# Optimization experiments

Hardware: AMD Instinct MI355X
Metric: run time of the kernel (lower is better)

## Reference

```python
import jax, jax.numpy as jnp
import numpy as np

B, S, D, H = 2, 2048, 1024, 16
DK = D // H  # 64


def setup_inputs() -> dict:
    key = jax.random.key(0)
    ks = jax.random.split(key, 9)
    s = 0.02
    return {
        "embeddings": jax.random.normal(ks[0], (B, S, D), jnp.float32),
        "Wq": jax.random.normal(ks[1], (H, D, DK), jnp.float32) * s,
        "bq": jax.random.normal(ks[2], (H, DK), jnp.float32) * s,
        "Wk": jax.random.normal(ks[3], (H, D, DK), jnp.float32) * s,
        "bk": jax.random.normal(ks[4], (H, DK), jnp.float32) * s,
        "Wv": jax.random.normal(ks[5], (H, D, DK), jnp.float32) * s,
        "bv": jax.random.normal(ks[6], (H, DK), jnp.float32) * s,
        "Wo": jax.random.normal(ks[7], (D, D), jnp.float32) * s,
        "bo": jax.random.normal(ks[8], (D,), jnp.float32) * s,
    }


def reference(embeddings, Wq, bq, Wk, bk, Wv, bv, Wo, bo):
    b, s, d = embeddings.shape
    dk = Wq.shape[-1]
    # batched per-head projections: [b,s,d] x [h,d,k] -> [b,h,s,k]
    q = jnp.einsum('bsd,hdk->bhsk', embeddings, Wq) + bq[None, :, None, :]
    k = jnp.einsum('bsd,hdk->bhsk', embeddings, Wk) + bk[None, :, None, :]
    v = jnp.einsum('bsd,hdk->bhsk', embeddings, Wv) + bv[None, :, None, :]
    scores = jnp.einsum('bhqk,bhsk->bhqs', q, k) / jnp.sqrt(jnp.float32(dk))
    causal_mask = jnp.triu(jnp.ones((s, s), dtype=bool), k=1)  # True above diagonal
    scores = jnp.where(causal_mask, jnp.float32(-1e9), scores)
    weights = jax.nn.softmax(scores, axis=-1)
    ctx = jnp.einsum('bhqs,bhsk->bhqk', weights, v)
    concat = ctx.transpose(0, 2, 1, 3).reshape(b, s, d)  # head-major concat, matches torch.cat
    return concat @ Wo + bo
```

## Files before the change

kernel.cpp:

```cpp
#include <hip/hip_runtime.h>
#include <hip/hip_bf16.h>

typedef unsigned short u16;
typedef unsigned int u32;
typedef __bf16 bf16x8 __attribute__((ext_vector_type(8)));
typedef float f32x4 __attribute__((ext_vector_type(4)));
typedef float f32x16 __attribute__((ext_vector_type(16)));

#define AS1 __attribute__((address_space(1)))
#define AS3 __attribute__((address_space(3)))

#define NB 2
#define NS 2048
#define ND 1024
#define NH 16
#define NK 64

__device__ __forceinline__ u16 f2bf(float f) {
  u32 u = __builtin_bit_cast(u32, f);
  return (u16)((u + 0x7FFFu + ((u >> 16) & 1u)) >> 16);
}

__device__ __forceinline__ u32 cvt_pk_bf16(float lo, float hi) {
  u32 u;
  asm("v_cvt_pk_bf16_f32 %0, %1, %2" : "=v"(u) : "v"(lo), "v"(hi));
  return u;
}

__device__ __forceinline__ void stage_tile(u16* lds, const u16* __restrict__ src, int rs,
                                           int wid, int lane) {
#pragma unroll
  for (int i = 0; i < 2; ++i) {
    int c = wid * 128 + i * 64 + lane;
    int row = c >> 3;
    int kc = (c & 7) ^ (row & 7);
    __builtin_amdgcn_global_load_lds((const AS1 u32*)(src + (size_t)row * rs + kc * 8),
                                     (AS3 u32*)(lds + (wid * 128 + i * 64) * 8), 16, 0, 0);
  }
}

__device__ __forceinline__ void stage_warp(u16* lds, const u16* __restrict__ src, int rs,
                                           int lane) {
#pragma unroll
  for (int i = 0; i < 8; ++i) {
    int c = i * 64 + lane;
    int row = c >> 3;
    int kc = (c & 7) ^ (row & 7);
    __builtin_amdgcn_global_load_lds((const AS1 u32*)(src + (size_t)row * rs + kc * 8),
                                     (AS3 u32*)(lds + i * 512), 16, 0, 0);
  }
}

__device__ __forceinline__ bf16x8 read_slot(const u16* lds, int row, int slot) {
  return *(const bf16x8*)(lds + row * 64 + (slot ^ (row & 7)) * 8);
}

__device__ __forceinline__ bf16x8 read_frag(const u16* lds, int row, int ks, int lane) {
  int slot = ((lane >> 4) + ks * 4) ^ (row & 7);
  return *(const bf16x8*)(lds + row * 64 + slot * 8);
}

__global__ __launch_bounds__(256) void convert_kernel(const float* __restrict__ src,
                                                      u16* __restrict__ dst, int n) {
  int i = (blockIdx.x * 256 + threadIdx.x) * 4;
  if (i >= n) return;
  float4 v = *(const float4*)(src + i);
  u32 w0 = cvt_pk_bf16(v.x, v.y);
  u32 w1 = cvt_pk_bf16(v.z, v.w);
  uint2 w; w.x = w0; w.y = w1;
  *(uint2*)(dst + i) = w;
}

__global__ __launch_bounds__(256) void transpose_conv(const float* __restrict__ src,
                                                      u16* __restrict__ dst, int R, int C) {
  __shared__ float tile[32][33];
  size_t base = (size_t)blockIdx.z * R * C;
  src += base;
  dst += base;
  int c0 = blockIdx.x * 32, r0 = blockIdx.y * 32;
  int tx = threadIdx.x, ty = threadIdx.y;
#pragma unroll
  for (int i = 0; i < 4; ++i)
    tile[ty + 8 * i][tx] = src[(size_t)(r0 + ty + 8 * i) * C + c0 + tx];
  __syncthreads();
#pragma unroll
  for (int i = 0; i < 4; ++i)
    dst[(size_t)(c0 + ty + 8 * i) * R + r0 + tx] = f2bf(tile[tx][ty + 8 * i]);
}

template <int MODE>
__global__ __launch_bounds__(256) void gemm128(const u16* __restrict__ A,
                                               const u16* __restrict__ Bt,
                                               const float* __restrict__ b0,
                                               const float* __restrict__ b1,
                                               const float* __restrict__ b2,
                                               u16* __restrict__ Qo, u16* __restrict__ Ko,
                                               u16* __restrict__ Vo,
                                               float* __restrict__ out) {
  __shared__ alignas(16) u16 lds_a[128 * 64];
  __shared__ alignas(16) u16 lds_b[128 * 64];
  int tid = threadIdx.x, lane = tid & 63, wid = tid >> 6;
  int wm = wid >> 1, wn = wid & 1;
  int m0 = blockIdx.x * 128, n0 = blockIdx.y * 128;
  int col = lane & 15;
  f32x4 zero4 = {0.f, 0.f, 0.f, 0.f};
  f32x4 acc[4][4];
#pragma unroll
  for (int i = 0; i < 4; ++i)
#pragma unroll
    for (int j = 0; j < 4; ++j) acc[i][j] = zero4;
  for (int k0 = 0; k0 < ND; k0 += 64) {
    stage_tile(lds_a, A + (size_t)m0 * ND + k0, ND, wid, lane);
    stage_tile(lds_a + 4096, A + (size_t)(m0 + 64) * ND + k0, ND, wid, lane);
    stage_tile(lds_b, Bt + (size_t)n0 * ND + k0, ND, wid, lane);
    stage_tile(lds_b + 4096, Bt + (size_t)(n0 + 64) * ND + k0, ND, wid, lane);
    __syncthreads();
#pragma unroll
    for (int ks = 0; ks < 2; ++ks) {
      bf16x8 af[4], bf[4];
#pragma unroll
      for (int i = 0; i < 4; ++i) af[i] = read_frag(lds_a, wm * 64 + i * 16 + col, ks, lane);
#pragma unroll
      for (int j = 0; j < 4; ++j) bf[j] = read_frag(lds_b, wn * 64 + j * 16 + col, ks, lane);
#pragma unroll
      for (int i = 0; i < 4; ++i)
#pragma unroll
        for (int j = 0; j < 4; ++j)
          acc[i][j] = __builtin_amdgcn_mfma_f32_16x16x32_bf16(af[i], bf[j], acc[i][j], 0, 0, 0);
    }
    __syncthreads();
  }
  int rbase = m0 + wm * 64 + (lane >> 4) * 4;
#pragma unroll
  for (int j = 0; j < 4; ++j) {
    int n = n0 + wn * 64 + j * 16 + col;
    if constexpr (MODE == 0) {
      int which = n >> 10, hh = (n >> 6) & 15, dk = n & 63;
      const float* bp = which == 0 ? b0 : which == 1 ? b1 : b2;
      float bn = bp[hh * 64 + dk];
      if (which == 0) {
#pragma unroll
        for (int i = 0; i < 4; ++i)
#pragma unroll
          for (int r = 0; r < 4; ++r) {
            int m = rbase + i * 16 + r;
            int bb = m >> 11, s = m & (NS - 1);
            Qo[((size_t)(bb * NH + hh) * NS + s) * NK + dk] =
                f2bf((acc[i][j][r] + bn) * 0.18033688f);
          }
      } else if (which == 1) {
#pragma unroll
        for (int i = 0; i < 4; ++i)
#pragma unroll
          for (int r = 0; r < 4; ++r) {
            int m = rbase + i * 16 + r;
            int bb = m >> 11, s = m & (NS - 1);
            Ko[((size_t)(bb * NH + hh) * NS + s) * NK + dk] = f2bf(acc[i][j][r] + bn);
          }
      } else {
#pragma unroll
        for (int i = 0; i < 4; ++i)
#pragma unroll
          for (int r = 0; r < 4; ++r) {
            int m = rbase + i * 16 + r;
            int bb = m >> 11, s = m & (NS - 1);
            int ss = (s & ~12) | ((s & 4) << 1) | ((s & 8) >> 1);
            Vo[((size_t)(bb * NH + hh) * NK + dk) * NS + ss] = f2bf(acc[i][j][r] + bn);
          }
      }
    } else {
      float bn = b0[n];
#pragma unroll
      for (int i = 0; i < 4; ++i)
#pragma unroll
        for (int r = 0; r < 4; ++r)
          out[(size_t)(rbase + i * 16 + r) * ND + n] = acc[i][j][r] + bn;
    }
  }
}

__global__ __launch_bounds__(128, 2) void attn_kernel(const u16* __restrict__ Q,
                                                      const u16* __restrict__ K,
                                                      const u16* __restrict__ Vt,
                                                      u16* __restrict__ ctx) {
  __shared__ alignas(16) u16 lds[2][2][8192];
  __shared__ float slab[2][32];
  int tid = threadIdx.x, lane = tid & 63, w = tid >> 6;
  int hi = lane >> 5, ln = lane & 31;
  int bh = blockIdx.x;
  int pr = blockIdx.y;
  const u16* Qb = Q + bh * (NS * NK);
  const u16* Kb = K + bh * (NS * NK);
  const u16* Vb = Vt + bh * (NK * NS);
  int b = bh >> 4, h = bh & 15;
  u16* myK0 = &lds[w][0][0];
  u16* myV0 = &lds[w][0][4096];
  u16* myK1 = &lds[w][1][0];
  u16* myV1 = &lds[w][1][4096];

#pragma unroll 1
  for (int half = 0; half < 2; ++half) {
    int qt = half ? pr : (31 - pr);
    int q0w = qt * 64 + w * 32;
    int qg = q0w + ln;
    bf16x8 qf[4];
#pragma unroll
    for (int ks = 0; ks < 4; ++ks)
      qf[ks] = *(const bf16x8*)(Qb + qg * NK + ks * 16 + hi * 8);

    f32x16 acc0, acc1;
#pragma unroll
    for (int r = 0; r < 16; ++r) { acc0[r] = 0.f; acc1[r] = 0.f; }
    float lp = 0.f;
    int nt = qt + 1;

    stage_warp(myK0, Kb, NK, lane);
    stage_warp(myV0, Vb, NS, lane);
    if (nt > 1) {
      stage_warp(myK1, Kb + 64 * NK, NK, lane);
      stage_warp(myV1, Vb + 64, NS, lane);
    }

#pragma unroll 1
    for (int t = 0; t < nt; ++t) {
      const u16* lk = (t & 1) ? myK1 : myK0;
      const u16* lv = (t & 1) ? myV1 : myV0;
      if (t + 1 < nt) {
        asm volatile("s_waitcnt vmcnt(16)" ::: "memory");
      } else {
        asm volatile("s_waitcnt vmcnt(0)" ::: "memory");
      }
      __builtin_amdgcn_sched_barrier(0);
      f32x16 sc0, sc1;
#pragma unroll
      for (int r = 0; r < 16; ++r) { sc0[r] = 0.f; sc1[r] = 0.f; }
      __builtin_amdgcn_s_setprio(1);
#pragma unroll
      for (int ks = 0; ks < 4; ++ks) {
        bf16x8 kf0 = read_slot(lk, ln, 2 * ks + hi);
        sc0 = __builtin_amdgcn_mfma_f32_32x32x16_bf16(kf0, qf[ks], sc0, 0, 0, 0);
        bf16x8 kf1 = read_slot(lk, 32 + ln, 2 * ks + hi);
        sc1 = __builtin_amdgcn_mfma_f32_32x32x16_bf16(kf1, qf[ks], sc1, 0, 0, 0);
      }
      __builtin_amdgcn_s_setprio(0);
      if (t == qt) {
#pragma unroll
        for (int r = 0; r < 16; ++r) {
          int kl = t * 64 + (r & 3) + 8 * (r >> 2) + 4 * hi;
          if (kl > qg) sc0[r] = -1e30f;
          if (kl + 32 > qg) sc1[r] = -1e30f;
        }
      }
      float ps[4] = {0.f, 0.f, 0.f, 0.f};
#pragma unroll
      for (int r = 0; r < 16; ++r) {
        float p = exp2f(sc0[r]);
        sc0[r] = p;
        ps[r & 3] += p;
      }
#pragma unroll
      for (int r = 0; r < 16; ++r) {
        float p = exp2f(sc1[r]);
        sc1[r] = p;
        ps[r & 3] += p;
      }
      lp += (ps[0] + ps[1]) + (ps[2] + ps[3]);
      u32 wd[8];
      bf16x8 pa[4];
#pragma unroll
      for (int i = 0; i < 8; ++i) wd[i] = cvt_pk_bf16(sc0[2 * i], sc0[2 * i + 1]);
      { uint4 q4; q4.x = wd[0]; q4.y = wd[1]; q4.z = wd[2]; q4.w = wd[3];
        pa[0] = __builtin_bit_cast(bf16x8, q4);
        q4.x = wd[4]; q4.y = wd[5]; q4.z = wd[6]; q4.w = wd[7];
        pa[1] = __builtin_bit_cast(bf16x8, q4); }
#pragma unroll
      for (int i = 0; i < 8; ++i) wd[i] = cvt_pk_bf16(sc1[2 * i], sc1[2 * i + 1]);
      { uint4 q4; q4.x = wd[0]; q4.y = wd[1]; q4.z = wd[2]; q4.w = wd[3];
        pa[2] = __builtin_bit_cast(bf16x8, q4);
        q4.x = wd[4]; q4.y = wd[5]; q4.z = wd[6]; q4.w = wd[7];
        pa[3] = __builtin_bit_cast(bf16x8, q4); }
      __builtin_amdgcn_s_setprio(1);
#pragma unroll
      for (int ks = 0; ks < 4; ++ks) {
        bf16x8 vf0 = read_slot(lv, ln, 2 * ks + hi);
        acc0 = __builtin_amdgcn_mfma_f32_32x32x16_bf16(pa[ks], vf0, acc0, 0, 0, 0);
        bf16x8 vf1 = read_slot(lv, 32 + ln, 2 * ks + hi);
        acc1 = __builtin_amdgcn_mfma_f32_32x32x16_bf16(pa[ks], vf1, acc1, 0, 0, 0);
      }
      __builtin_amdgcn_s_setprio(0);
      if (t + 2 < nt) {
        asm volatile("s_waitcnt lgkmcnt(0)" ::: "memory");
        __builtin_amdgcn_sched_barrier(0);
        u16* nk = (t & 1) ? myK1 : myK0;
        u16* nv = (t & 1) ? myV1 : myV0;
        stage_warp(nk, Kb + (t + 2) * 64 * NK, NK, lane);
        stage_warp(nv, Vb + (t + 2) * 64, NS, lane);
      }
    }
    lp += __shfl_xor(lp, 32);
    if (!hi) slab[w][ln] = 1.0f / lp;
    float iv[16];
#pragma unroll
    for (int r = 0; r < 16; ++r) iv[r] = slab[w][(r & 3) + 8 * (r >> 2) + 4 * hi];
#pragma unroll
    for (int r = 0; r < 16; ++r) {
      int qq = q0w + (r & 3) + 8 * (r >> 2) + 4 * hi;
      size_t base = (size_t)(b * NS + qq) * ND + h * NK + ln;
      ctx[base] = f2bf(acc0[r] * iv[r]);
      ctx[base + 32] = f2bf(acc1[r] * iv[r]);
    }
  }
}

extern "C" void kernel_launch(void* const* d_in, const int* in_sizes, int n_in,
                              void* d_out, int out_size, void* d_ws, size_t ws_size,
                              hipStream_t stream) {
  (void)in_sizes; (void)n_in; (void)out_size;
  const float* emb = (const float*)d_in[0];
  const float* Wq = (const float*)d_in[1];
  const float* bq = (const float*)d_in[2];
  const float* Wk = (const float*)d_in[3];
  const float* bk = (const float*)d_in[4];
  const float* Wv = (const float*)d_in[5];
  const float* bv = (const float*)d_in[6];
  const float* Wo = (const float*)d_in[7];
  const float* bo = (const float*)d_in[8];
  float* out = (float*)d_out;

  const size_t EMB_N = (size_t)NB * NS * ND;
  const size_t W_N = (size_t)NH * ND * NK;
  const size_t QKV_N = (size_t)NB * NH * NS * NK;
  if (ws_size < (EMB_N + 4 * W_N + 3 * QKV_N) * sizeof(u16)) return;
  u16* ws = (u16*)d_ws;
  u16* emb_bf = ws;
  u16* Wqt = emb_bf + EMB_N;
  u16* Wkt = Wqt + W_N;
  u16* Wvt = Wkt + W_N;
  u16* Wot = Wvt + W_N;
  u16* Qb = Wot + W_N;
  u16* Kb = Qb + QKV_N;
  u16* Vtb = Kb + QKV_N;
  u16* ctxb = emb_bf;

  convert_kernel<<<dim3((int)(EMB_N / 4 / 256)), dim3(256), 0, stream>>>(emb, emb_bf,
                                                                         (int)EMB_N);
  dim3 tb(32, 8);
  transpose_conv<<<dim3(2, 32, 16), tb, 0, stream>>>(Wq, Wqt, ND, NK);
  transpose_conv<<<dim3(2, 32, 16), tb, 0, stream>>>(Wk, Wkt, ND, NK);
  transpose_conv<<<dim3(2, 32, 16), tb, 0, stream>>>(Wv, Wvt, ND, NK);
  transpose_conv<<<dim3(32, 32, 1), tb, 0, stream>>>(Wo, Wot, ND, ND);
  gemm128<0><<<dim3(32, 24), dim3(256), 0, stream>>>(emb_bf, Wqt, bq, bk, bv, Qb, Kb, Vtb,
                                                     nullptr);
  attn_kernel<<<dim3(32, 16), dim3(128), 0, stream>>>(Qb, Kb, Vtb, ctxb);
  gemm128<1><<<dim3(32, 8), dim3(256), 0, stream>>>(ctxb, Wot, bo, nullptr, nullptr,
                                                    nullptr, nullptr, nullptr, out);
}
```

Before: 141.6 us.

## Launch one block per query tile and load V fragments directly from global

Drops the paired heavy/light causal tile scheme: each block now handles a single query tile, and the grid doubles to 32x32 blocks. V is no longer staged in LDS. Each iteration loads V fragments straight from global memory into registers, which halves LDS use and shortens the vmcnt wait. The aim is more blocks in flight and less LDS traffic. The cost is load imbalance across causal tiles and V reads from global that may be less coalesced, with their latency exposed in the loop.

```diff
diff --git a/kernel.cpp b/kernel.cpp
--- a/kernel.cpp
+++ b/kernel.cpp
@@ -183,132 +183,123 @@
                                                       const u16* __restrict__ K,
                                                       const u16* __restrict__ Vt,
                                                       u16* __restrict__ ctx) {
-  __shared__ alignas(16) u16 lds[2][2][8192];
+  __shared__ alignas(16) u16 ldsK[2][2][4096];
   __shared__ float slab[2][32];
   int tid = threadIdx.x, lane = tid & 63, w = tid >> 6;
   int hi = lane >> 5, ln = lane & 31;
   int bh = blockIdx.x;
-  int pr = blockIdx.y;
+  int qt = blockIdx.y;
   const u16* Qb = Q + bh * (NS * NK);
   const u16* Kb = K + bh * (NS * NK);
   const u16* Vb = Vt + bh * (NK * NS);
   int b = bh >> 4, h = bh & 15;
-  u16* myK0 = &lds[w][0][0];
-  u16* myV0 = &lds[w][0][4096];
-  u16* myK1 = &lds[w][1][0];
-  u16* myV1 = &lds[w][1][4096];
+  u16* myK0 = &ldsK[w][0][0];
+  u16* myK1 = &ldsK[w][1][0];
+
+  int q0w = qt * 64 + w * 32;
+  int qg = q0w + ln;
+  bf16x8 qf[4];
+#pragma unroll
+  for (int ks = 0; ks < 4; ++ks)
+    qf[ks] = *(const bf16x8*)(Qb + qg * NK + ks * 16 + hi * 8);
+
+  f32x16 acc0, acc1;
+#pragma unroll
+  for (int r = 0; r < 16; ++r) { acc0[r] = 0.f; acc1[r] = 0.f; }
+  float lp = 0.f;
+  int nt = qt + 1;
+
+  stage_warp(myK0, Kb, NK, lane);
+  if (nt > 1) stage_warp(myK1, Kb + 64 * NK, NK, lane);
 
 #pragma unroll 1
-  for (int half = 0; half < 2; ++half) {
-    int qt = half ? pr : (31 - pr);
-    int q0w = qt * 64 + w * 32;
-    int qg = q0w + ln;
-    bf16x8 qf[4];
-#pragma unroll
-    for (int ks = 0; ks < 4; ++ks)
-      qf[ks] = *(const bf16x8*)(Qb + qg * NK + ks * 16 + hi * 8);
-
-    f32x16 acc0, acc1;
-#pragma unroll
-    for (int r = 0; r < 16; ++r) { acc0[r] = 0.f; acc1[r] = 0.f; }
-    float lp = 0.f;
-    int nt = qt + 1;
-
-    stage_warp(myK0, Kb, NK, lane);
-    stage_warp(myV0, Vb, NS, lane);
-    if (nt > 1) {
-      stage_warp(myK1, Kb + 64 * NK, NK, lane);
-      stage_warp(myV1, Vb + 64, NS, lane);
-    }
-
-#pragma unroll 1
-    for (int t = 0; t < nt; ++t) {
-      const u16* lk = (t & 1) ? myK1 : myK0;
-      const u16* lv = (t & 1) ? myV1 : myV0;
-      if (t + 1 < nt) {
-        asm volatile("s_waitcnt vmcnt(16)" ::: "memory");
-      } else {
-        asm volatile("s_waitcnt vmcnt(0)" ::: "memory");
+  for (int t = 0; t < nt; ++t) {
+    const u16* lk = (t & 1) ? myK1 : myK0;
+    if (t + 1 < nt) {
+      asm volatile("s_waitcnt vmcnt(8)" ::: "memory");
+    } else {
+      asm volatile("s_waitcnt vmcnt(0)" ::: "memory");
+    }
+    __builtin_amdgcn_sched_barrier(0);
+    const u16* Vtb_ = Vb + t * 64;
+    bf16x8 vf0[4], vf1[4];
+#pragma unroll
+    for (int ks = 0; ks < 4; ++ks) {
+      vf0[ks] = *(const bf16x8*)(Vtb_ + (size_t)ln * NS + (2 * ks + hi) * 8);
+      vf1[ks] = *(const bf16x8*)(Vtb_ + (size_t)(32 + ln) * NS + (2 * ks + hi) * 8);
+    }
+    f32x16 sc0, sc1;
+#pragma unroll
+    for (int r = 0; r < 16; ++r) { sc0[r] = 0.f; sc1[r] = 0.f; }
+    __builtin_amdgcn_s_setprio(1);
+#pragma unroll
+    for (int ks = 0; ks < 4; ++ks) {
+      bf16x8 kf0 = read_slot(lk, ln, 2 * ks + hi);
+      sc0 = __builtin_amdgcn_mfma_f32_32x32x16_bf16(kf0, qf[ks], sc0, 0, 0, 0);
+      bf16x8 kf1 = read_slot(lk, 32 + ln, 2 * ks + hi);
+      sc1 = __builtin_amdgcn_mfma_f32_32x32x16_bf16(kf1, qf[ks], sc1, 0, 0, 0);
+    }
+    __builtin_amdgcn_s_setprio(0);
+    if (t == qt) {
+#pragma unroll
+      for (int r = 0; r < 16; ++r) {
+        int kl = t * 64 + (r & 3) + 8 * (r >> 2) + 4 * hi;
+        if (kl > qg) sc0[r] = -1e30f;
+        if (kl + 32 > qg) sc1[r] = -1e30f;
       }
+    }
+    float ps[4] = {0.f, 0.f, 0.f, 0.f};
+#pragma unroll
+    for (int r = 0; r < 16; ++r) {
+      float p = exp2f(sc0[r]);
+      sc0[r] = p;
+      ps[r & 3] += p;
+    }
+#pragma unroll
+    for (int r = 0; r < 16; ++r) {
+      float p = exp2f(sc1[r]);
+      sc1[r] = p;
+      ps[r & 3] += p;
+    }
+    lp += (ps[0] + ps[1]) + (ps[2] + ps[3]);
+    u32 wd[8];
+    bf16x8 pa[4];
+#pragma unroll
+    for (int i = 0; i < 8; ++i) wd[i] = cvt_pk_bf16(sc0[2 * i], sc0[2 * i + 1]);
+    { uint4 q4; q4.x = wd[0]; q4.y = wd[1]; q4.z = wd[2]; q4.w = wd[3];
+      pa[0] = __builtin_bit_cast(bf16x8, q4);
+      q4.x = wd[4]; q4.y = wd[5]; q4.z = wd[6]; q4.w = wd[7];
+      pa[1] = __builtin_bit_cast(bf16x8, q4); }
+#pragma unroll
+    for (int i = 0; i < 8; ++i) wd[i] = cvt_pk_bf16(sc1[2 * i], sc1[2 * i + 1]);
+    { uint4 q4; q4.x = wd[0]; q4.y = wd[1]; q4.z = wd[2]; q4.w = wd[3];
+      pa[2] = __builtin_bit_cast(bf16x8, q4);
+      q4.x = wd[4]; q4.y = wd[5]; q4.z = wd[6]; q4.w = wd[7];
+      pa[3] = __builtin_bit_cast(bf16x8, q4); }
+    __builtin_amdgcn_s_setprio(1);
+#pragma unroll
+    for (int ks = 0; ks < 4; ++ks) {
+      acc0 = __builtin_amdgcn_mfma_f32_32x32x16_bf16(pa[ks], vf0[ks], acc0, 0, 0, 0);
+      acc1 = __builtin_amdgcn_mfma_f32_32x32x16_bf16(pa[ks], vf1[ks], acc1, 0, 0, 0);
+    }
+    __builtin_amdgcn_s_setprio(0);
+    if (t + 2 < nt) {
+      asm volatile("s_waitcnt lgkmcnt(0)" ::: "memory");
       __builtin_amdgcn_sched_barrier(0);
-      f32x16 sc0, sc1;
-#pragma unroll
-      for (int r = 0; r < 16; ++r) { sc0[r] = 0.f; sc1[r] = 0.f; }
-      __builtin_amdgcn_s_setprio(1);
-#pragma unroll
-      for (int ks = 0; ks < 4; ++ks) {
-        bf16x8 kf0 = read_slot(lk, ln, 2 * ks + hi);
-        sc0 = __builtin_amdgcn_mfma_f32_32x32x16_bf16(kf0, qf[ks], sc0, 0, 0, 0);
-        bf16x8 kf1 = read_slot(lk, 32 + ln, 2 * ks + hi);
-        sc1 = __builtin_amdgcn_mfma_f32_32x32x16_bf16(kf1, qf[ks], sc1, 0, 0, 0);
-      }
-      __builtin_amdgcn_s_setprio(0);
-      if (t == qt) {
-#pragma unroll
-        for (int r = 0; r < 16; ++r) {
-          int kl = t * 64 + (r & 3) + 8 * (r >> 2) + 4 * hi;
-          if (kl > qg) sc0[r] = -1e30f;
-          if (kl + 32 > qg) sc1[r] = -1e30f;
-        }
-      }
-      float ps[4] = {0.f, 0.f, 0.f, 0.f};
-#pragma unroll
-      for (int r = 0; r < 16; ++r) {
-        float p = exp2f(sc0[r]);
-        sc0[r] = p;
-        ps[r & 3] += p;
-      }
-#pragma unroll
-      for (int r = 0; r < 16; ++r) {
-        float p = exp2f(sc1[r]);
-        sc1[r] = p;
-        ps[r & 3] += p;
-      }
-      lp += (ps[0] + ps[1]) + (ps[2] + ps[3]);
-      u32 wd[8];
-      bf16x8 pa[4];
-#pragma unroll
-      for (int i = 0; i < 8; ++i) wd[i] = cvt_pk_bf16(sc0[2 * i], sc0[2 * i + 1]);
-      { uint4 q4; q4.x = wd[0]; q4.y = wd[1]; q4.z = wd[2]; q4.w = wd[3];
-        pa[0] = __builtin_bit_cast(bf16x8, q4);
-        q4.x = wd[4]; q4.y = wd[5]; q4.z = wd[6]; q4.w = wd[7];
-        pa[1] = __builtin_bit_cast(bf16x8, q4); }
-#pragma unroll
-      for (int i = 0; i < 8; ++i) wd[i] = cvt_pk_bf16(sc1[2 * i], sc1[2 * i + 1]);
-      { uint4 q4; q4.x = wd[0]; q4.y = wd[1]; q4.z = wd[2]; q4.w = wd[3];
-        pa[2] = __builtin_bit_cast(bf16x8, q4);
-        q4.x = wd[4]; q4.y = wd[5]; q4.z = wd[6]; q4.w = wd[7];
-        pa[3] = __builtin_bit_cast(bf16x8, q4); }
-      __builtin_amdgcn_s_setprio(1);
-#pragma unroll
-      for (int ks = 0; ks < 4; ++ks) {
-        bf16x8 vf0 = read_slot(lv, ln, 2 * ks + hi);
-        acc0 = __builtin_amdgcn_mfma_f32_32x32x16_bf16(pa[ks], vf0, acc0, 0, 0, 0);
-        bf16x8 vf1 = read_slot(lv, 32 + ln, 2 * ks + hi);
-        acc1 = __builtin_amdgcn_mfma_f32_32x32x16_bf16(pa[ks], vf1, acc1, 0, 0, 0);
-      }
-      __builtin_amdgcn_s_setprio(0);
-      if (t + 2 < nt) {
-        asm volatile("s_waitcnt lgkmcnt(0)" ::: "memory");
-        __builtin_amdgcn_sched_barrier(0);
-        u16* nk = (t & 1) ? myK1 : myK0;
-        u16* nv = (t & 1) ? myV1 : myV0;
-        stage_warp(nk, Kb + (t + 2) * 64 * NK, NK, lane);
-        stage_warp(nv, Vb + (t + 2) * 64, NS, lane);
-      }
-    }
-    lp += __shfl_xor(lp, 32);
-    if (!hi) slab[w][ln] = 1.0f / lp;
-    float iv[16];
-#pragma unroll
-    for (int r = 0; r < 16; ++r) iv[r] = slab[w][(r & 3) + 8 * (r >> 2) + 4 * hi];
-#pragma unroll
-    for (int r = 0; r < 16; ++r) {
-      int qq = q0w + (r & 3) + 8 * (r >> 2) + 4 * hi;
-      size_t base = (size_t)(b * NS + qq) * ND + h * NK + ln;
-      ctx[base] = f2bf(acc0[r] * iv[r]);
-      ctx[base + 32] = f2bf(acc1[r] * iv[r]);
-    }
+      stage_warp((t & 1) ? myK1 : myK0, Kb + (t + 2) * 64 * NK, NK, lane);
+    }
+  }
+  lp += __shfl_xor(lp, 32);
+  if (!hi) slab[w][ln] = 1.0f / lp;
+  float iv[16];
+#pragma unroll
+  for (int r = 0; r < 16; ++r) iv[r] = slab[w][(r & 3) + 8 * (r >> 2) + 4 * hi];
+#pragma unroll
+  for (int r = 0; r < 16; ++r) {
+    int qq = q0w + (r & 3) + 8 * (r >> 2) + 4 * hi;
+    size_t base = (size_t)(b * NS + qq) * ND + h * NK + ln;
+    ctx[base] = f2bf(acc0[r] * iv[r]);
+    ctx[base + 32] = f2bf(acc1[r] * iv[r]);
   }
 }
 
@@ -351,7 +342,7 @@
   transpose_conv<<<dim3(32, 32, 1), tb, 0, stream>>>(Wo, Wot, ND, ND);
   gemm128<0><<<dim3(32, 24), dim3(256), 0, stream>>>(emb_bf, Wqt, bq, bk, bv, Qb, Kb, Vtb,
                                                      nullptr);
-  attn_kernel<<<dim3(32, 16), dim3(128), 0, stream>>>(Qb, Kb, Vtb, ctxb);
+  attn_kernel<<<dim3(32, 32), dim3(128), 0, stream>>>(Qb, Kb, Vtb, ctxb);
   gemm128<1><<<dim3(32, 8), dim3(256), 0, stream>>>(ctxb, Wot, bo, nullptr, nullptr,
                                                     nullptr, nullptr, nullptr, out);
 }
```

Measured after the change: 148.2 us. +4.7%, slower.
